# Kernel optimization log

Measured on AMD Instinct MI355X. Metric: run time of the kernel, lower is better.

## Reference

```python
import jax, jax.numpy as jnp
import numpy as np

N_NODES = 100000
N_EDGES = 1600000
D_IN = 128
HIDDEN = 128
EPS = 1e-5


def setup_inputs() -> dict:
    key = jax.random.key(0)
    ks = jax.random.split(key, 12)
    glorot = lambda k, o, i: jax.random.normal(k, (o, i), jnp.float32) * (2.0 / (o + i)) ** 0.5
    return {
        "x": jax.random.normal(ks[0], (N_NODES, D_IN), jnp.float32),
        "edge_index": jax.random.randint(ks[1], (2, N_EDGES), 0, N_NODES, jnp.int64),
        # SAGEConv layer 1: lin_l (neighbors, with bias), lin_r (root, no bias)
        "Wl1": glorot(ks[2], HIDDEN, D_IN),
        "bl1": jnp.zeros((HIDDEN,), jnp.float32),
        "Wr1": glorot(ks[3], HIDDEN, D_IN),
        # SAGEConv layer 2
        "Wl2": glorot(ks[4], HIDDEN, HIDDEN),
        "bl2": jnp.zeros((HIDDEN,), jnp.float32),
        "Wr2": glorot(ks[5], HIDDEN, HIDDEN),
        # BatchNorm1d affine params
        "gamma": jnp.ones((HIDDEN,), jnp.float32),
        "beta": jnp.zeros((HIDDEN,), jnp.float32),
        # final fc (xavier_uniform weight, zero bias per init_weights)
        "fcW": jax.random.uniform(ks[6], (HIDDEN, HIDDEN), jnp.float32, -1.0, 1.0) * (6.0 / (2 * HIDDEN)) ** 0.5,
        "fcb": jnp.zeros((HIDDEN,), jnp.float32),
    }


def _sage_conv(h, src, dst, n, Wl, bl, Wr):
    # mean-aggregate neighbor features: scatter x[src] onto dst
    msg_sum = jax.ops.segment_sum(h[src], dst, num_segments=n)          # [N, F]
    deg = jax.ops.segment_sum(jnp.ones((src.shape[0],), h.dtype), dst, num_segments=n)
    agg = msg_sum / jnp.maximum(deg, 1.0)[:, None]
    return agg @ Wl.T + bl + h @ Wr.T


def reference(x, edge_index, Wl1, bl1, Wr1, Wl2, bl2, Wr2, gamma, beta, fcW, fcb):
    src, dst = edge_index[0], edge_index[1]
    n = x.shape[0]
    h = jax.nn.relu(_sage_conv(x, src, dst, n, Wl1, bl1, Wr1))  # inter-layer relu in PyG BasicGNN
    h = _sage_conv(h, src, dst, n, Wl2, bl2, Wr2)
    h = jax.nn.relu(h)
    # BatchNorm1d, training-mode (batch stats, biased variance)
    mu = h.mean(axis=0)
    var = ((h - mu) ** 2).mean(axis=0)
    h = (h - mu) * jax.lax.rsqrt(var + EPS) * gamma + beta
    # dropout p=0.0 -> identity
    return h @ fcW.T + fcb
```

## Files before the change

kernel.cpp:

```cpp
#include <hip/hip_runtime.h>
#include <hip/hip_bf16.h>

#define D 128
#define EPSV 1e-5f
#define BSH 7
#define BWIDTH 128
#define NCB 256
#define MAXBUCK 1024

typedef __attribute__((ext_vector_type(8))) short bf16x8;
typedef __attribute__((ext_vector_type(4))) float f32x4;
typedef unsigned short u16;

__device__ inline u16 f2bf(float f) {
    unsigned int u = __builtin_bit_cast(unsigned int, f);
    return (u16)((u + 0x7fffu + ((u >> 16) & 1u)) >> 16);
}
__device__ inline float bf2f(u16 u) {
    unsigned int x = ((unsigned int)u) << 16;
    return __builtin_bit_cast(float, x);
}

__device__ inline void gl_lds16(const void* g, void* l) {
    __builtin_amdgcn_global_load_lds(
        (const __attribute__((address_space(1))) unsigned int*)g,
        (__attribute__((address_space(3))) unsigned int*)l,
        16, 0, 0);
}

__global__ void k_cvt(const float* __restrict__ in, u16* __restrict__ out, long long n8) {
    long long i = (long long)blockIdx.x * blockDim.x + threadIdx.x;
    long long stride = (long long)gridDim.x * blockDim.x;
    for (; i < n8; i += stride) {
        const float4 v0 = *(const float4*)(in + i * 8);
        const float4 v1 = *(const float4*)(in + i * 8 + 4);
        bf16x8 o;
        o[0] = (short)f2bf(v0.x); o[1] = (short)f2bf(v0.y);
        o[2] = (short)f2bf(v0.z); o[3] = (short)f2bf(v0.w);
        o[4] = (short)f2bf(v1.x); o[5] = (short)f2bf(v1.y);
        o[6] = (short)f2bf(v1.z); o[7] = (short)f2bf(v1.w);
        *(bf16x8*)(out + i * 8) = o;
    }
}

__global__ __launch_bounds__(256) void k_cvt4(const float* __restrict__ s0, const float* __restrict__ s1,
                                              const float* __restrict__ s2, const float* __restrict__ s3,
                                              u16* __restrict__ out) {
    int i = blockIdx.x * 256 + threadIdx.x;
    int mat = i >> 11;
    int off = (i & 2047) * 8;
    const float* src = (mat == 0) ? s0 : (mat == 1) ? s1 : (mat == 2) ? s2 : s3;
    const float4 v0 = *(const float4*)(src + off);
    const float4 v1 = *(const float4*)(src + off + 4);
    bf16x8 o;
    o[0] = (short)f2bf(v0.x); o[1] = (short)f2bf(v0.y);
    o[2] = (short)f2bf(v0.z); o[3] = (short)f2bf(v0.w);
    o[4] = (short)f2bf(v1.x); o[5] = (short)f2bf(v1.y);
    o[6] = (short)f2bf(v1.z); o[7] = (short)f2bf(v1.w);
    *(bf16x8*)(out + (size_t)i * 8) = o;
}

__global__ __launch_bounds__(256) void k_bhist(const int* __restrict__ dst, int E, int chunk,
                                               int nbuck, int* __restrict__ bh) {
    __shared__ int h[MAXBUCK];
    int t = threadIdx.x;
    for (int i = t; i < nbuck; i += 256) h[i] = 0;
    __syncthreads();
    int beg = blockIdx.x * chunk, end = min(E, beg + chunk);
    for (int i = beg + t; i < end; i += 256) atomicAdd(&h[dst[i] >> BSH], 1);
    __syncthreads();
    for (int i = t; i < nbuck; i += 256) bh[(size_t)blockIdx.x * nbuck + i] = h[i];
}

__global__ __launch_bounds__(NCB) void k_colscan(int* __restrict__ bh, int nbuck, int* __restrict__ btot) {
    __shared__ int sm[NCB];
    int b = blockIdx.x;
    int t = threadIdx.x;
    int v = bh[(size_t)t * nbuck + b];
    sm[t] = v;
    __syncthreads();
    for (int off = 1; off < NCB; off <<= 1) {
        int a = (t >= off) ? sm[t - off] : 0;
        __syncthreads();
        sm[t] += a;
        __syncthreads();
    }
    bh[(size_t)t * nbuck + b] = sm[t] - v;
    if (t == NCB - 1) btot[b] = sm[t];
}

__global__ __launch_bounds__(1024) void k_btotscan(const int* __restrict__ btot, int nbuck,
                                                   int* __restrict__ bbase, int* __restrict__ row_ptr,
                                                   int M, int E) {
    __shared__ int sm[1024];
    int t = threadIdx.x;
    int v = (t < nbuck) ? btot[t] : 0;
    sm[t] = v;
    __syncthreads();
    for (int off = 1; off < 1024; off <<= 1) {
        int a = (t >= off) ? sm[t - off] : 0;
        __syncthreads();
        sm[t] += a;
        __syncthreads();
    }
    if (t < nbuck) bbase[t] = sm[t] - v;
    if (t == 0) { bbase[nbuck] = E; row_ptr[M] = E; }
}

__global__ __launch_bounds__(256) void k_bfill(const int* __restrict__ src, const int* __restrict__ dst,
                                               int E, int chunk, int nbuck, const int* __restrict__ bh,
                                               const int* __restrict__ bbase, unsigned int* __restrict__ pairs) {
    __shared__ int cur[MAXBUCK];
    int t = threadIdx.x;
    for (int i = t; i < nbuck; i += 256)
        cur[i] = bbase[i] + bh[(size_t)blockIdx.x * nbuck + i];
    __syncthreads();
    int beg = blockIdx.x * chunk, end = min(E, beg + chunk);
    for (int i = beg + t; i < end; i += 256) {
        int d = dst[i];
        int bk = d >> BSH;
        int pos = atomicAdd(&cur[bk], 1);
        pairs[pos] = (unsigned int)src[i] | ((unsigned int)(d & (BWIDTH - 1)) << 24);
    }
}

__global__ __launch_bounds__(256) void k_b2csr(const unsigned int* __restrict__ pairs,
                                               const int* __restrict__ bbase, int nbuck, int M,
                                               int* __restrict__ row_ptr, int* __restrict__ csr) {
    __shared__ int nh[BWIDTH];
    __shared__ int sc[BWIDTH];
    __shared__ int nc[BWIDTH];
    int b = blockIdx.x;
    int t = threadIdx.x;
    int node0 = b << BSH;
    int beg = bbase[b], end = bbase[b + 1];
    if (t < BWIDTH) nh[t] = 0;
    __syncthreads();
    for (int i = beg + t; i < end; i += 256) atomicAdd(&nh[pairs[i] >> 24], 1);
    __syncthreads();
    if (t < BWIDTH) sc[t] = nh[t];
    __syncthreads();
    for (int off = 1; off < BWIDTH; off <<= 1) {
        int a = 0;
        if (t < BWIDTH && t >= off) a = sc[t - off];
        __syncthreads();
        if (t < BWIDTH) sc[t] += a;
        __syncthreads();
    }
    if (t < BWIDTH) {
        int ex = sc[t] - nh[t];
        nc[t] = ex;
        int node = node0 + t;
        if (node < M) row_ptr[node] = beg + ex;
    }
    __syncthreads();
    for (int i = beg + t; i < end; i += 256) {
        unsigned int p = pairs[i];
        int pos = atomicAdd(&nc[p >> 24], 1);
        csr[beg + pos] = (int)(p & 0xFFFFFFu);
    }
}

__global__ __launch_bounds__(256) void k_gather(const u16* __restrict__ feat, const int* __restrict__ rp,
                                                const int* __restrict__ csr, u16* __restrict__ msg, int M) {
    int sub = threadIdx.x & 15;
    int node = blockIdx.x * 16 + (threadIdx.x >> 4);
    if (node >= M) return;
    int beg = rp[node], end = rp[node + 1];
    float a0[8], a1[8], a2[8], a3[8];
    #pragma unroll
    for (int j = 0; j < 8; j++) { a0[j] = 0.f; a1[j] = 0.f; a2[j] = 0.f; a3[j] = 0.f; }
    int e = beg;
    for (; e + 7 < end; e += 8) {
        int s0 = csr[e], s1 = csr[e + 1], s2 = csr[e + 2], s3 = csr[e + 3];
        int s4 = csr[e + 4], s5 = csr[e + 5], s6 = csr[e + 6], s7 = csr[e + 7];
        bf16x8 v0 = *(const bf16x8*)(feat + (size_t)s0 * D + sub * 8);
        bf16x8 v1 = *(const bf16x8*)(feat + (size_t)s1 * D + sub * 8);
        bf16x8 v2 = *(const bf16x8*)(feat + (size_t)s2 * D + sub * 8);
        bf16x8 v3 = *(const bf16x8*)(feat + (size_t)s3 * D + sub * 8);
        bf16x8 v4 = *(const bf16x8*)(feat + (size_t)s4 * D + sub * 8);
        bf16x8 v5 = *(const bf16x8*)(feat + (size_t)s5 * D + sub * 8);
        bf16x8 v6 = *(const bf16x8*)(feat + (size_t)s6 * D + sub * 8);
        bf16x8 v7 = *(const bf16x8*)(feat + (size_t)s7 * D + sub * 8);
        #pragma unroll
        for (int j = 0; j < 8; j++) {
            a0[j] += bf2f((u16)v0[j]); a1[j] += bf2f((u16)v1[j]);
            a2[j] += bf2f((u16)v2[j]); a3[j] += bf2f((u16)v3[j]);
            a0[j] += bf2f((u16)v4[j]); a1[j] += bf2f((u16)v5[j]);
            a2[j] += bf2f((u16)v6[j]); a3[j] += bf2f((u16)v7[j]);
        }
    }
    for (; e + 3 < end; e += 4) {
        int s0 = csr[e], s1 = csr[e + 1], s2 = csr[e + 2], s3 = csr[e + 3];
        bf16x8 v0 = *(const bf16x8*)(feat + (size_t)s0 * D + sub * 8);
        bf16x8 v1 = *(const bf16x8*)(feat + (size_t)s1 * D + sub * 8);
        bf16x8 v2 = *(const bf16x8*)(feat + (size_t)s2 * D + sub * 8);
        bf16x8 v3 = *(const bf16x8*)(feat + (size_t)s3 * D + sub * 8);
        #pragma unroll
        for (int j = 0; j < 8; j++) {
            a0[j] += bf2f((u16)v0[j]); a1[j] += bf2f((u16)v1[j]);
            a2[j] += bf2f((u16)v2[j]); a3[j] += bf2f((u16)v3[j]);
        }
    }
    for (; e < end; e++) {
        bf16x8 v0 = *(const bf16x8*)(feat + (size_t)csr[e] * D + sub * 8);
        #pragma unroll
        for (int j = 0; j < 8; j++) a0[j] += bf2f((u16)v0[j]);
    }
    float inv = 1.0f / fmaxf((float)(end - beg), 1.0f);
    bf16x8 o;
    #pragma unroll
    for (int j = 0; j < 8; j++) o[j] = (short)f2bf((a0[j] + a1[j] + a2[j] + a3[j]) * inv);
    *(bf16x8*)(msg + (size_t)node * D + sub * 8) = o;
}

template <int TWO, int RELU, int OUTBF>
__global__ __launch_bounds__(256) void k_gemm(
    const u16* __restrict__ A1, const u16* __restrict__ A2,
    const u16* __restrict__ W1b, const u16* __restrict__ W2b,
    const float* __restrict__ bias, void* __restrict__ Cout,
    int M, int nstrips) {
    constexpr int NOPS = TWO ? 2 : 1;
    __shared__ __align__(16) u16 lds[NOPS * 16384 + 2 * NOPS * 8192];
    u16* wlds = lds;
    u16* alds = lds + NOPS * 16384;

    int t = threadIdx.x;
    int lane = t & 63, wave = t >> 6;
    int rlo = lane & 15, khi = lane >> 4;

    auto stage = [&](int buf, int sidx) {
        int rsub = khi;
        #pragma unroll
        for (int c = 0; c < 4; c++) {
            int chunk = wave * 4 + c;
            int lrow = chunk * 4 + rsub;
            int ra = sidx * 64 + lrow;
            if (ra > M - 1) ra = M - 1;
            int src16 = rlo ^ (lrow & 7);
            gl_lds16(A1 + (size_t)ra * D + src16 * 8,
                     alds + ((size_t)buf * NOPS + 0) * 8192 + chunk * 512);
            if (TWO)
                gl_lds16(A2 + (size_t)ra * D + src16 * 8,
                         alds + ((size_t)buf * NOPS + 1) * 8192 + chunk * 512);
        }
    };

    int s0 = blockIdx.x;
    if (s0 < nstrips) stage(0, s0);

    {
        const int nrows = NOPS * 128;
        for (int idx = t; idx < nrows; idx += 256) {
            int mat = idx >> 7, row = idx & 127;
            const u16* g = (mat ? W2b : W1b) + (size_t)row * D;
            u16* base = wlds + mat * 16384 + row * D;
            #pragma unroll
            for (int c16 = 0; c16 < 16; c16++) {
                bf16x8 v = *(const bf16x8*)(g + c16 * 8);
                *(bf16x8*)(base + ((c16 ^ (row & 7)) * 8)) = v;
            }
        }
    }
    __syncthreads();

    int cur = 0;
    for (int s = s0; s < nstrips; s += gridDim.x) {
        int nxt = s + gridDim.x;
        if (nxt < nstrips) stage(cur ^ 1, nxt);

        int r_local = wave * 16 + rlo;
        bf16x8 af[NOPS][4];
        #pragma unroll
        for (int o = 0; o < NOPS; o++) {
            const u16* ab = alds + ((size_t)cur * NOPS + o) * 8192 + r_local * D;
            #pragma unroll
            for (int kk = 0; kk < 4; kk++)
                af[o][kk] = *(const bf16x8*)(ab + (((kk * 4 + khi) ^ (r_local & 7)) * 8));
        }

        f32x4 acc[8];
        #pragma unroll
        for (int nt = 0; nt < 8; nt++) acc[nt] = (f32x4){0.f, 0.f, 0.f, 0.f};

        #pragma unroll
        for (int nt = 0; nt < 8; nt++) {
            int row = nt * 16 + rlo;
            #pragma unroll
            for (int o = 0; o < NOPS; o++) {
                const u16* wb = wlds + o * 16384 + (size_t)row * D;
                bf16x8 wf[4];
                #pragma unroll
                for (int kk = 0; kk < 4; kk++)
                    wf[kk] = *(const bf16x8*)(wb + (((kk * 4 + khi) ^ (row & 7)) * 8));
                #pragma unroll
                for (int kk = 0; kk < 4; kk++)
                    acc[nt] = __builtin_amdgcn_mfma_f32_16x16x32_bf16(af[o][kk], wf[kk], acc[nt], 0, 0, 0);
            }
        }

        int mrow0 = s * 64 + wave * 16 + khi * 4;
        #pragma unroll
        for (int nt = 0; nt < 8; nt++) {
            int col = nt * 16 + rlo;
            float bn = bias[col];
            #pragma unroll
            for (int r = 0; r < 4; r++) {
                int row = mrow0 + r;
                if (row < M) {
                    float v = acc[nt][r] + bn;
                    if (RELU) v = fmaxf(v, 0.0f);
                    if (OUTBF) ((u16*)Cout)[(size_t)row * D + col] = f2bf(v);
                    else       ((float*)Cout)[(size_t)row * D + col] = v;
                }
            }
        }

        asm volatile("s_waitcnt vmcnt(32)" ::: "memory");
        __syncthreads();
        cur ^= 1;
    }
}

__global__ __launch_bounds__(256) void k_bnstats(const u16* __restrict__ h, int M, float* __restrict__ stats) {
    __shared__ float ssum[256];
    __shared__ float ssq[256];
    int col = threadIdx.x & 127;
    int half = threadIdx.x >> 7;
    float s = 0.f, s2 = 0.f;
    for (int r = blockIdx.x * 2 + half; r < M; r += 512) {
        float v = bf2f(h[(size_t)r * D + col]);
        s += v;
        s2 += v * v;
    }
    ssum[threadIdx.x] = s;
    ssq[threadIdx.x] = s2;
    __syncthreads();
    if (threadIdx.x < 128) {
        unsafeAtomicAdd(&stats[col], ssum[threadIdx.x] + ssum[threadIdx.x + 128]);
        unsafeAtomicAdd(&stats[128 + col], ssq[threadIdx.x] + ssq[threadIdx.x + 128]);
    }
}

__global__ __launch_bounds__(128) void k_bnfold(const float* __restrict__ stats,
                                                const float* __restrict__ gamma, const float* __restrict__ beta,
                                                const float* __restrict__ fcW, const float* __restrict__ fcb,
                                                int M, u16* __restrict__ Wfold, float* __restrict__ bias2) {
    __shared__ float red[128];
    int n = blockIdx.x, t = threadIdx.x;
    float mu = stats[t] / (float)M;
    float var = stats[128 + t] / (float)M - mu * mu;
    float sc = gamma[t] * rsqrtf(var + EPSV);
    float sh = beta[t] - mu * sc;
    float w = fcW[(size_t)n * D + t];
    Wfold[(size_t)n * D + t] = f2bf(w * sc);
    red[t] = sh * w;
    __syncthreads();
    for (int off = 64; off > 0; off >>= 1) {
        if (t < off) red[t] += red[t + off];
        __syncthreads();
    }
    if (t == 0) bias2[n] = fcb[n] + red[0];
}

static inline size_t alup(size_t x) { return (x + 63) & ~(size_t)63; }

extern "C" void kernel_launch(void* const* d_in, const int* in_sizes, int n_in,
                              void* d_out, int out_size, void* d_ws, size_t ws_size,
                              hipStream_t stream) {
    const float* x   = (const float*)d_in[0];
    const int*   ei  = (const int*)d_in[1];
    const float* Wl1 = (const float*)d_in[2];
    const float* bl1 = (const float*)d_in[3];
    const float* Wr1 = (const float*)d_in[4];
    const float* Wl2 = (const float*)d_in[5];
    const float* bl2 = (const float*)d_in[6];
    const float* Wr2 = (const float*)d_in[7];
    const float* gamma = (const float*)d_in[8];
    const float* beta  = (const float*)d_in[9];
    const float* fcW = (const float*)d_in[10];
    const float* fcb = (const float*)d_in[11];
    float* out = (float*)d_out;

    const int M = in_sizes[0] / D;
    const int E = in_sizes[1] / 2;
    const int* srcI = ei;
    const int* dstI = ei + E;
    const int nbuck = (M + BWIDTH - 1) >> BSH;
    const int chunk = (E + NCB - 1) / NCB;

    char* p = (char*)d_ws;
    u16* xb   = (u16*)p;            p += alup((size_t)M * D * 2);
    u16* msgb = (u16*)p;            p += alup((size_t)M * D * 2);
    u16* h1b  = (u16*)p;            p += alup((size_t)M * D * 2);
    u16* h2b  = (u16*)p;            p += alup((size_t)M * D * 2);
    unsigned int* pairs = (unsigned int*)p; p += alup((size_t)E * 4);
    int* csr  = (int*)p;            p += alup((size_t)E * 4);
    int* row_ptr = (int*)p;         p += alup((size_t)(M + 1) * 4);
    int* bh   = (int*)p;            p += alup((size_t)NCB * nbuck * 4);
    int* btot = (int*)p;            p += alup((size_t)nbuck * 4);
    int* bbase= (int*)p;            p += alup((size_t)(nbuck + 1) * 4);
    float* stats = (float*)p;       p += alup(256 * 4);
    u16* Wb   = (u16*)p;            p += alup((size_t)4 * D * D * 2);
    u16* Wfoldb = (u16*)p;          p += alup((size_t)D * D * 2);
    float* bias2 = (float*)p;       p += alup(128 * 4);

    u16* Wl1b = Wb;
    u16* Wr1b = Wb + 16384;
    u16* Wl2b = Wb + 32768;
    u16* Wr2b = Wb + 49152;

    const int nstrips = (M + 63) / 64;
    const int GG2 = 256;
    const int GG1 = 512;
    const int gather_grid = (M + 15) / 16;

    hipMemsetAsync(stats, 0, 256 * sizeof(float), stream);

    k_cvt<<<2048, 256, 0, stream>>>(x, xb, (long long)M * D / 8);
    k_cvt4<<<32, 256, 0, stream>>>(Wl1, Wr1, Wl2, Wr2, Wb);
    k_bhist<<<NCB, 256, 0, stream>>>(dstI, E, chunk, nbuck, bh);
    k_colscan<<<nbuck, NCB, 0, stream>>>(bh, nbuck, btot);
    k_btotscan<<<1, 1024, 0, stream>>>(btot, nbuck, bbase, row_ptr, M, E);
    k_bfill<<<NCB, 256, 0, stream>>>(srcI, dstI, E, chunk, nbuck, bh, bbase, pairs);
    k_b2csr<<<nbuck, 256, 0, stream>>>(pairs, bbase, nbuck, M, row_ptr, csr);

    k_gather<<<gather_grid, 256, 0, stream>>>(xb, row_ptr, csr, msgb, M);
    k_gemm<1, 1, 1><<<GG2, 256, 0, stream>>>(msgb, xb, Wl1b, Wr1b, bl1, h1b, M, nstrips);

    k_gather<<<gather_grid, 256, 0, stream>>>(h1b, row_ptr, csr, msgb, M);
    k_gemm<1, 1, 1><<<GG2, 256, 0, stream>>>(msgb, h1b, Wl2b, Wr2b, bl2, h2b, M, nstrips);

    k_bnstats<<<256, 256, 0, stream>>>(h2b, M, stats);
    k_bnfold<<<128, 128, 0, stream>>>(stats, gamma, beta, fcW, fcb, M, Wfoldb, bias2);

    k_gemm<0, 0, 0><<<GG1, 256, 0, stream>>>(h2b, nullptr, Wfoldb, nullptr, bias2, out, M, nstrips);
}
```

Baseline: 436.3 us.

## Replace LDS-staged persistent GEMM with register-resident weights and direct global A loads

```diff
diff --git a/kernel.cpp b/kernel.cpp
--- a/kernel.cpp
+++ b/kernel.cpp
@@ -19,13 +19,6 @@
 __device__ inline float bf2f(u16 u) {
     unsigned int x = ((unsigned int)u) << 16;
     return __builtin_bit_cast(float, x);
-}
-
-__device__ inline void gl_lds16(const void* g, void* l) {
-    __builtin_amdgcn_global_load_lds(
-        (const __attribute__((address_space(1))) unsigned int*)g,
-        (__attribute__((address_space(3))) unsigned int*)l,
-        16, 0, 0);
 }
 
 __global__ void k_cvt(const float* __restrict__ in, u16* __restrict__ out, long long n8) {
@@ -218,107 +211,62 @@
 __global__ __launch_bounds__(256) void k_gemm(
     const u16* __restrict__ A1, const u16* __restrict__ A2,
     const u16* __restrict__ W1b, const u16* __restrict__ W2b,
-    const float* __restrict__ bias, void* __restrict__ Cout,
-    int M, int nstrips) {
+    const float* __restrict__ bias, void* __restrict__ Cout, int M) {
     constexpr int NOPS = TWO ? 2 : 1;
-    __shared__ __align__(16) u16 lds[NOPS * 16384 + 2 * NOPS * 8192];
-    u16* wlds = lds;
-    u16* alds = lds + NOPS * 16384;
-
     int t = threadIdx.x;
     int lane = t & 63, wave = t >> 6;
     int rlo = lane & 15, khi = lane >> 4;
-
-    auto stage = [&](int buf, int sidx) {
-        int rsub = khi;
-        #pragma unroll
-        for (int c = 0; c < 4; c++) {
-            int chunk = wave * 4 + c;
-            int lrow = chunk * 4 + rsub;
-            int ra = sidx * 64 + lrow;
-            if (ra > M - 1) ra = M - 1;
-            int src16 = rlo ^ (lrow & 7);
-            gl_lds16(A1 + (size_t)ra * D + src16 * 8,
-                     alds + ((size_t)buf * NOPS + 0) * 8192 + chunk * 512);
-            if (TWO)
-                gl_lds16(A2 + (size_t)ra * D + src16 * 8,
-                         alds + ((size_t)buf * NOPS + 1) * 8192 + chunk * 512);
-        }
-    };
-
-    int s0 = blockIdx.x;
-    if (s0 < nstrips) stage(0, s0);
-
-    {
-        const int nrows = NOPS * 128;
-        for (int idx = t; idx < nrows; idx += 256) {
-            int mat = idx >> 7, row = idx & 127;
-            const u16* g = (mat ? W2b : W1b) + (size_t)row * D;
-            u16* base = wlds + mat * 16384 + row * D;
+    int m0 = blockIdx.x * 64;
+
+    bf16x8 wf[NOPS][2][4];
+    #pragma unroll
+    for (int j = 0; j < 2; j++) {
+        int wrow = (wave * 2 + j) * 16 + rlo;
+        #pragma unroll
+        for (int kk = 0; kk < 4; kk++) {
+            wf[0][j][kk] = *(const bf16x8*)(W1b + (size_t)wrow * D + kk * 32 + khi * 8);
+            if (TWO) wf[1][j][kk] = *(const bf16x8*)(W2b + (size_t)wrow * D + kk * 32 + khi * 8);
+        }
+    }
+    float bn0 = bias[(wave * 2 + 0) * 16 + rlo];
+    float bn1 = bias[(wave * 2 + 1) * 16 + rlo];
+
+    #pragma unroll
+    for (int mt = 0; mt < 4; mt++) {
+        int ra = m0 + mt * 16 + rlo;
+        if (ra > M - 1) ra = M - 1;
+        bf16x8 af[NOPS][4];
+        #pragma unroll
+        for (int kk = 0; kk < 4; kk++) {
+            af[0][kk] = *(const bf16x8*)(A1 + (size_t)ra * D + kk * 32 + khi * 8);
+            if (TWO) af[1][kk] = *(const bf16x8*)(A2 + (size_t)ra * D + kk * 32 + khi * 8);
+        }
+        f32x4 acc0 = (f32x4){0.f, 0.f, 0.f, 0.f};
+        f32x4 acc1 = (f32x4){0.f, 0.f, 0.f, 0.f};
+        #pragma unroll
+        for (int o = 0; o < NOPS; o++)
             #pragma unroll
-            for (int c16 = 0; c16 < 16; c16++) {
-                bf16x8 v = *(const bf16x8*)(g + c16 * 8);
-                *(bf16x8*)(base + ((c16 ^ (row & 7)) * 8)) = v;
+            for (int kk = 0; kk < 4; kk++) {
+                acc0 = __builtin_amdgcn_mfma_f32_16x16x32_bf16(af[o][kk], wf[o][0][kk], acc0, 0, 0, 0);
+                acc1 = __builtin_amdgcn_mfma_f32_16x16x32_bf16(af[o][kk], wf[o][1][kk], acc1, 0, 0, 0);
             }
-        }
-    }
-    __syncthreads();
-
-    int cur = 0;
-    for (int s = s0; s < nstrips; s += gridDim.x) {
-        int nxt = s + gridDim.x;
-        if (nxt < nstrips) stage(cur ^ 1, nxt);
-
-        int r_local = wave * 16 + rlo;
-        bf16x8 af[NOPS][4];
-        #pragma unroll
-        for (int o = 0; o < NOPS; o++) {
-            const u16* ab = alds + ((size_t)cur * NOPS + o) * 8192 + r_local * D;
-            #pragma unroll
-            for (int kk = 0; kk < 4; kk++)
-                af[o][kk] = *(const bf16x8*)(ab + (((kk * 4 + khi) ^ (r_local & 7)) * 8));
-        }
-
-        f32x4 acc[8];
-        #pragma unroll
-        for (int nt = 0; nt < 8; nt++) acc[nt] = (f32x4){0.f, 0.f, 0.f, 0.f};
-
-        #pragma unroll
-        for (int nt = 0; nt < 8; nt++) {
-            int row = nt * 16 + rlo;
-            #pragma unroll
-            for (int o = 0; o < NOPS; o++) {
-                const u16* wb = wlds + o * 16384 + (size_t)row * D;
-                bf16x8 wf[4];
-                #pragma unroll
-                for (int kk = 0; kk < 4; kk++)
-                    wf[kk] = *(const bf16x8*)(wb + (((kk * 4 + khi) ^ (row & 7)) * 8));
-                #pragma unroll
-                for (int kk = 0; kk < 4; kk++)
-                    acc[nt] = __builtin_amdgcn_mfma_f32_16x16x32_bf16(af[o][kk], wf[kk], acc[nt], 0, 0, 0);
-            }
-        }
-
-        int mrow0 = s * 64 + wave * 16 + khi * 4;
-        #pragma unroll
-        for (int nt = 0; nt < 8; nt++) {
-            int col = nt * 16 + rlo;
-            float bn = bias[col];
+        int row0 = m0 + mt * 16 + khi * 4;
+        #pragma unroll
+        for (int j = 0; j < 2; j++) {
+            int col = (wave * 2 + j) * 16 + rlo;
+            float bn = j ? bn1 : bn0;
+            f32x4 a = j ? acc1 : acc0;
             #pragma unroll
             for (int r = 0; r < 4; r++) {
-                int row = mrow0 + r;
+                int row = row0 + r;
                 if (row < M) {
-                    float v = acc[nt][r] + bn;
+                    float v = a[r] + bn;
                     if (RELU) v = fmaxf(v, 0.0f);
                     if (OUTBF) ((u16*)Cout)[(size_t)row * D + col] = f2bf(v);
                     else       ((float*)Cout)[(size_t)row * D + col] = v;
                 }
             }
         }
-
-        asm volatile("s_waitcnt vmcnt(32)" ::: "memory");
-        __syncthreads();
-        cur ^= 1;
     }
 }
 
@@ -410,9 +358,7 @@
     u16* Wl2b = Wb + 32768;
     u16* Wr2b = Wb + 49152;
 
-    const int nstrips = (M + 63) / 64;
-    const int GG2 = 256;
-    const int GG1 = 512;
+    const int gemm_grid = (M + 63) / 64;
     const int gather_grid = (M + 15) / 16;
 
     hipMemsetAsync(stats, 0, 256 * sizeof(float), stream);
@@ -426,13 +372,13 @@
     k_b2csr<<<nbuck, 256, 0, stream>>>(pairs, bbase, nbuck, M, row_ptr, csr);
 
     k_gather<<<gather_grid, 256, 0, stream>>>(xb, row_ptr, csr, msgb, M);
-    k_gemm<1, 1, 1><<<GG2, 256, 0, stream>>>(msgb, xb, Wl1b, Wr1b, bl1, h1b, M, nstrips);
+    k_gemm<1, 1, 1><<<gemm_grid, 256, 0, stream>>>(msgb, xb, Wl1b, Wr1b, bl1, h1b, M);
 
     k_gather<<<gather_grid, 256, 0, stream>>>(h1b, row_ptr, csr, msgb, M);
-    k_gemm<1, 1, 1><<<GG2, 256, 0, stream>>>(msgb, h1b, Wl2b, Wr2b, bl2, h2b, M, nstrips);
+    k_gemm<1, 1, 1><<<gemm_grid, 256, 0, stream>>>(msgb, h1b, Wl2b, Wr2b, bl2, h2b, M);
 
     k_bnstats<<<256, 256, 0, stream>>>(h2b, M, stats);
     k_bnfold<<<128, 128, 0, stream>>>(stats, gamma, beta, fcW, fcb, M, Wfoldb, bias2);
 
-    k_gemm<0, 0, 0><<<GG1, 256, 0, stream>>>(h2b, nullptr, Wfoldb, nullptr, bias2, out, M, nstrips);
-}
+    k_gemm<0, 0, 0><<<gemm_grid, 256, 0, stream>>>(h2b, nullptr, Wfoldb, nullptr, bias2, out, M);
+}
```

After: 474.8 us. 1.09x slower.
